# Kernel tuning notes

Hardware: AMD Instinct MI355X
Metric: run time of the kernel (lower is better)

## Reference

```python
import jax, jax.numpy as jnp
import numpy as np

B, E, H, DEPTH = 8192, 512, 512, 1


def setup_inputs() -> dict:
    key = jax.random.key(0)
    ks = jax.random.split(key, 10)
    inp = {
        "X": jax.random.normal(ks[0], (B, E), jnp.float32),
        "prev_a": jax.random.normal(ks[1], (B, DEPTH + 1, H), jnp.float32),
        "prev_b": jax.random.normal(ks[2], (B, DEPTH + 1, H), jnp.float32),
        "prev_depth": jax.random.randint(ks[3], (B, 1), 0, DEPTH + 1, jnp.int32),
        # torch.nn.Linear weights, shape [out, in], y = x @ W.T
        "w_f": jax.random.normal(ks[4], (1, H), jnp.float32) * 0.02,
        "w_a00": jax.random.normal(ks[5], (H, E + H), jnp.float32) * 0.02,
        "w_a10": jax.random.normal(ks[6], (H, E + H), jnp.float32) * 0.02,
        "w_b00": jax.random.normal(ks[7], (H, E + 2 * H), jnp.float32) * 0.02,
        "w_b11": jax.random.normal(ks[8], (H, E + H), jnp.float32) * 0.02,
        "w_b10": jax.random.normal(ks[9], (H, E + H), jnp.float32) * 0.02,
    }
    return inp


def reference(X, prev_a, prev_b, prev_depth, w_f, w_a00, w_a10, w_b00, w_b11, w_b10):
    dt = X.dtype
    # gather prev_b at current depth per batch row: prev_b[b, prev_depth[b,0], :]
    b_top = jnp.take_along_axis(prev_b, prev_depth[:, :, None], axis=1)[:, 0, :]  # [B,H]
    # fork decision; torch rounds then casts to long -> no grad flows through w_f
    f_raw = jax.lax.stop_gradient(jnp.round(jax.nn.sigmoid(b_top @ w_f.T)))  # [B,1]
    all_zero = jnp.all(prev_depth == 0)
    f = jnp.where(all_zero, jnp.ones_like(f_raw), f_raw)
    j = jnp.where(all_zero, jnp.zeros_like(f_raw), f_raw)  # else-branch sets j = f
    next_depth = prev_depth + (f - j).astype(prev_depth.dtype)  # [B,1]

    d = 1  # depth fixed to 1
    pa, pb0, pb1 = prev_a[:, d, :], prev_b[:, d - 1, :], prev_b[:, d, :]

    fj, nn_, fn = f * j, (1.0 - f) * (1.0 - j), f * (1.0 - j)  # [B,1] gates
    eq = (next_depth == d).astype(dt)
    lt = (next_depth < d).astype(dt)

    nofork_nojoin_a = jnp.concatenate([X, pa], 1) @ w_a00.T
    fork_nojoin_a = jnp.concatenate([X, pb0], 1) @ w_a10.T
    next_a1 = eq * (fj * pa + nn_ * nofork_nojoin_a + fn * fork_nojoin_a) + lt * pa

    fork_join_b = jnp.concatenate([X, pb1], 1) @ w_b11.T
    nofork_nojoin_b = jnp.concatenate([X, pa, next_a1], 1) @ w_b00.T
    fork_nojoin_b = jnp.concatenate([X, next_a1], 1) @ w_b10.T
    next_b1 = eq * (fj * fork_join_b + nn_ * nofork_nojoin_b + fn * fork_nojoin_b) + lt * pb1

    zeros = jnp.zeros_like(next_a1)
    next_a = jnp.stack([zeros, next_a1], 1)  # [B, 2, H]
    next_b = jnp.stack([zeros, next_b1], 1)  # [B, 2, H]
    return next_a, next_b, next_depth, f, j
```

## Files before the change

kernel.cpp:

```cpp
#include <hip/hip_runtime.h>
#include <hip/hip_bf16.h>

typedef __attribute__((ext_vector_type(8))) __bf16 bf16x8;
typedef __attribute__((ext_vector_type(4))) float f32x4;
typedef __attribute__((ext_vector_type(4))) unsigned short u16x4;
typedef unsigned short u16;
typedef unsigned long long u64;

typedef __attribute__((address_space(1))) void gvoid;
typedef __attribute__((address_space(3))) void lvoid;

#define B_DIM 8192
#define MFMA(a, b, c) __builtin_amdgcn_mfma_f32_16x16x32_bf16((a), (b), (c), 0, 0, 0)

__device__ __forceinline__ u16x4 cvt4(f32x4 v) {
    u16x4 r;
    r.x = __builtin_bit_cast(u16, __float2bfloat16(v.x));
    r.y = __builtin_bit_cast(u16, __float2bfloat16(v.y));
    r.z = __builtin_bit_cast(u16, __float2bfloat16(v.z));
    r.w = __builtin_bit_cast(u16, __float2bfloat16(v.w));
    return r;
}

__device__ __forceinline__ void stage64(const u16* g, int ldg, u16* ls, int t) {
#pragma unroll
    for (int it = 0; it < 2; ++it) {
        int e = it * 2048 + t * 8;
        int r = e >> 6;
        int slot = (e & 63) >> 3;
        int csrc = (slot ^ (r & 7)) << 3;
        __builtin_amdgcn_global_load_lds((gvoid*)(g + (size_t)r * ldg + csrc),
                                         (lvoid*)&ls[e], 16, 0, 0);
    }
}

__device__ __forceinline__ bf16x8 ld_frag(const u16* ls, int row, int kslot) {
    return *(const bf16x8*)&ls[row * 64 + ((kslot ^ (row & 7)) << 3)];
}

__global__ void k_dots(const float* __restrict__ prev_b, const int* __restrict__ prev_depth,
                       const float* __restrict__ w_f,
                       const float* __restrict__ wa00f, const float* __restrict__ wa10f,
                       const float* __restrict__ wb00f, const float* __restrict__ wb11f,
                       const float* __restrict__ wb10f,
                       u16* __restrict__ wa00b, u16* __restrict__ wa10b,
                       u16* __restrict__ wb00b, u16* __restrict__ wb11b,
                       u16* __restrict__ wb10b,
                       float* __restrict__ dotv) {
    int blk = blockIdx.x;
    if (blk >= 2048) {
        int t = (blk - 2048) * 256 + threadIdx.x;
        const int S = 131072, SB = 196608;
        const float* src; u16* dst; int off;
        if      (t < S)            { src = wa00f; dst = wa00b; off = t; }
        else if (t < 2 * S)        { src = wa10f; dst = wa10b; off = t - S; }
        else if (t < 2 * S + SB)   { src = wb00f; dst = wb00b; off = t - 2 * S; }
        else if (t < 3 * S + SB)   { src = wb11f; dst = wb11b; off = t - 2 * S - SB; }
        else if (t < 4 * S + SB)   { src = wb10f; dst = wb10b; off = t - 3 * S - SB; }
        else return;
        f32x4 v = *(const f32x4*)(src + (size_t)off * 4);
        *(u16x4*)(dst + (size_t)off * 4) = cvt4(v);
        return;
    }
    int wv = threadIdx.x >> 6, l = threadIdx.x & 63;
    int row = blk * 4 + wv;
    int depth = prev_depth[row];
    const float* bt = prev_b + (size_t)row * 1024 + (size_t)depth * 512;
    const int i1 = l * 4, i2 = 256 + l * 4;
    f32x4 v0 = *(const f32x4*)(bt + i1);
    f32x4 v1 = *(const f32x4*)(bt + i2);
    f32x4 w0 = *(const f32x4*)(w_f + i1);
    f32x4 w1 = *(const f32x4*)(w_f + i2);
    float dot = v0.x*w0.x + v0.y*w0.y + v0.z*w0.z + v0.w*w0.w
              + v1.x*w1.x + v1.y*w1.y + v1.z*w1.z + v1.w*w1.w;
    for (int off = 32; off > 0; off >>= 1) dot += __shfl_xor(dot, off, 64);
    if (l == 0) dotv[row] = dot;
}

__global__ __launch_bounds__(1024) void k_scan(
        const float* __restrict__ dotv, const int* __restrict__ prev_depth,
        int* __restrict__ info, int* __restrict__ idx, int* __restrict__ cnt) {
    __shared__ u64 wtot[16];
    __shared__ int wany[16];
    const int tid = threadIdx.x, lane = tid & 63, wv = tid >> 6;
    int r0 = tid * 8;
    int dep[8]; float dv[8];
    int any = 0;
#pragma unroll
    for (int r = 0; r < 8; ++r) {
        dep[r] = prev_depth[r0 + r];
        dv[r] = dotv[r0 + r];
        any |= dep[r];
    }
    for (int off = 32; off > 0; off >>= 1) any |= __shfl_xor(any, off, 64);
    if (lane == 0) wany[wv] = any;
    __syncthreads();
    int ga = 0;
#pragma unroll
    for (int w = 0; w < 16; ++w) ga |= wany[w];
    int az = (ga == 0);

    int rcls[8], rf[8], rj[8], rnd[8];
    u64 pk = 0;
#pragma unroll
    for (int r = 0; r < 8; ++r) {
        float sg = 1.0f / (1.0f + expf(-dv[r]));
        int fi = (int)rintf(sg);
        int f = az ? 1 : fi;
        int j = az ? 0 : fi;
        int nd = dep[r] + f - j;
        int cls;
        if (nd == 1)     cls = f ? (j ? 2 : 1) : 0;
        else             cls = (nd < 1) ? 3 : 4;
        rcls[r] = cls; rf[r] = f; rj[r] = j; rnd[r] = nd;
        if (cls < 3) pk += 1ull << (cls * 21);
    }
    u64 own = pk;
    for (int off = 1; off < 64; off <<= 1) {
        u64 v = __shfl_up(pk, off, 64);
        if (lane >= off) pk += v;
    }
    if (lane == 63) wtot[wv] = pk;
    __syncthreads();
    u64 wbase = 0, tot = 0;
#pragma unroll
    for (int w = 0; w < 16; ++w) {
        u64 v = wtot[w];
        if (w < wv) wbase += v;
        tot += v;
    }
    u64 excl = wbase + pk - own;
    const u64 M21 = (1ull << 21) - 1;
    int tot0 = (int)(tot & M21), tot1 = (int)((tot >> 21) & M21), tot2 = (int)((tot >> 42) & M21);
    int base0 = 0;
    int base1 = (tot0 + 63) & ~63;
    int base2 = base1 + ((tot1 + 63) & ~63);
    int o0 = base0 + (int)(excl & M21);
    int o1 = base1 + (int)((excl >> 21) & M21);
    int o2 = base2 + (int)((excl >> 42) & M21);
#pragma unroll
    for (int r = 0; r < 8; ++r) {
        int row = r0 + r, cls = rcls[r], pos = 0;
        if (cls == 0)      { pos = o0++; idx[pos] = row; }
        else if (cls == 1) { pos = o1++; idx[pos] = row; }
        else if (cls == 2) { pos = o2++; idx[pos] = row; }
        info[row] = cls | (rf[r] << 3) | (rj[r] << 4) | (rnd[r] << 5) | (pos << 7);
    }
    if (tid < 64) {
        int p0 = tot0 + tid;          if (p0 < base1) idx[p0] = 0;
        int p1 = base1 + tot1 + tid;  if (p1 < base2) idx[p1] = 0;
        int end2 = base2 + ((tot2 + 63) & ~63);
        int p2 = base2 + tot2 + tid;  if (p2 < end2) idx[p2] = 0;
    }
    if (tid == 0) {
        cnt[0] = tot0; cnt[1] = tot1; cnt[2] = tot2;
        cnt[4] = base0; cnt[5] = base1; cnt[6] = base2;
    }
}

__global__ void k_mid(const float* __restrict__ X, const float* __restrict__ prev_a,
                      const float* __restrict__ prev_b,
                      const int* __restrict__ info, const int* __restrict__ idx,
                      const int* __restrict__ cnt,
                      u16* __restrict__ A_all,
                      float* __restrict__ outA, float* __restrict__ outB,
                      float* __restrict__ outD, float* __restrict__ outF,
                      float* __restrict__ outJ) {
    int blk = (int)blockIdx.x;
    int wv = threadIdx.x >> 6, l = threadIdx.x & 63;
    const int i1 = l * 4, i2 = 256 + l * 4;
    if (blk >= 2048) {
        int p = (blk - 2048) * 4 + wv;
        int base1 = cnt[5], base2 = cnt[6];
        int end2 = base2 + ((cnt[2] + 63) & ~63);
        if (p >= end2) return;
        const float* sec = (p < base1) ? (prev_a + 512)
                         : (p < base2) ? prev_b
                                       : (prev_b + 512);
        int row = idx[p];
        size_t r512 = (size_t)row * 512, r1024 = (size_t)row * 1024;
        f32x4 xa = *(const f32x4*)(X + r512 + i1);
        f32x4 xb = *(const f32x4*)(X + r512 + i2);
        f32x4 sa = *(const f32x4*)(sec + r1024 + i1);
        f32x4 sb = *(const f32x4*)(sec + r1024 + i2);
        size_t pbase = (size_t)p * 1024;
        *(u16x4*)(A_all + pbase + i1)       = cvt4(xa);
        *(u16x4*)(A_all + pbase + i2)       = cvt4(xb);
        *(u16x4*)(A_all + pbase + 512 + i1) = cvt4(sa);
        *(u16x4*)(A_all + pbase + 512 + i2) = cvt4(sb);
        return;
    }
    int row = blk * 4 + wv;
    int inf = info[row];
    int cls = inf & 7;
    size_t r1024 = (size_t)row * 1024;
    f32x4 z; z.x = 0.f; z.y = 0.f; z.z = 0.f; z.w = 0.f;
    *(f32x4*)(outA + r1024 + i1) = z;
    *(f32x4*)(outA + r1024 + i2) = z;
    *(f32x4*)(outB + r1024 + i1) = z;
    *(f32x4*)(outB + r1024 + i2) = z;
    if (l == 0) {
        outD[row] = (float)((inf >> 5) & 3);
        outF[row] = (float)((inf >> 3) & 1);
        outJ[row] = (float)((inf >> 4) & 1);
    }
    if (cls == 2 || cls == 3) {
        f32x4 pa0 = *(const f32x4*)(prev_a + r1024 + 512 + i1);
        f32x4 pa1 = *(const f32x4*)(prev_a + r1024 + 512 + i2);
        *(f32x4*)(outA + r1024 + 512 + i1) = pa0;
        *(f32x4*)(outA + r1024 + 512 + i2) = pa1;
        if (cls == 3) {
            f32x4 q10 = *(const f32x4*)(prev_b + r1024 + 512 + i1);
            f32x4 q11 = *(const f32x4*)(prev_b + r1024 + 512 + i2);
            *(f32x4*)(outB + r1024 + 512 + i1) = q10;
            *(f32x4*)(outB + r1024 + 512 + i2) = q11;
        }
    } else if (cls == 4) {
        *(f32x4*)(outA + r1024 + 512 + i1) = z;
        *(f32x4*)(outA + r1024 + 512 + i2) = z;
        *(f32x4*)(outB + r1024 + 512 + i1) = z;
        *(f32x4*)(outB + r1024 + 512 + i2) = z;
    }
}

__global__ __launch_bounds__(256, 4) void k_s1(
    const u16* __restrict__ A_all,
    const u16* __restrict__ wa00, const u16* __restrict__ wa10,
    const u16* __restrict__ wb00, const u16* __restrict__ wb11,
    const u16* __restrict__ wb10,
    const int* __restrict__ idx, const int* __restrict__ cnt,
    u16* __restrict__ na1_all, float* __restrict__ part,
    float* __restrict__ outA, float* __restrict__ outB)
{
    __shared__ u16 lsA[4096], lsB0[4096], lsB1[4096];
    int c0 = cnt[0], c1 = cnt[1], c2 = cnt[2];
    int base0 = cnt[4], base1 = cnt[5], base2 = cnt[6];
    int t0 = (c0 + 63) >> 6, t1 = (c1 + 63) >> 6, t2 = (c2 + 63) >> 6;
    int blk = (int)blockIdx.x;
    int T = blk >> 3, nt = blk & 7;
    int cls, mb, cc;
    const u16 *W0, *W1 = nullptr;
    int ldW1 = 0;
    if (T < t0)                { cls = 0; mb = base0 + T * 64; cc = c0; W0 = wa00; W1 = wb00; ldW1 = 1536; }
    else if (T < t0 + t1)      { T -= t0; cls = 1; mb = base1 + T * 64; cc = c1; W0 = wa10; W1 = wb10; ldW1 = 1024; }
    else if (T < t0 + t1 + t2) { T -= t0 + t1; cls = 2; mb = base2 + T * 64; cc = c2; W0 = wb11; }
    else return;
    const int t = threadIdx.x;
    const int n0 = nt * 64;
    const int lane = t & 63, wv = t >> 6;
    const int wr = (wv >> 1) * 32, wc = (wv & 1) * 32;
    const int fr = lane & 15, fq = lane >> 4;

    f32x4 acc0[2][2] = {}, acc1[2][2] = {};

    for (int kq = 0; kq < 16; ++kq) {
        int cb = kq * 64;
        stage64(A_all + (size_t)mb * 1024 + cb, 1024, lsA, t);
        stage64(W0 + (size_t)n0 * 1024 + cb, 1024, lsB0, t);
        bool dual = (cls == 0) || (cls == 1 && kq < 8);
        if (dual) stage64(W1 + (size_t)n0 * ldW1 + cb, ldW1, lsB1, t);
        __syncthreads();
#pragma unroll
        for (int kk = 0; kk < 2; ++kk) {
            int ks = kk * 4 + fq;
            bf16x8 a[2], b0[2], b1[2];
#pragma unroll
            for (int mi = 0; mi < 2; ++mi) a[mi] = ld_frag(lsA, wr + mi * 16 + fr, ks);
#pragma unroll
            for (int ni = 0; ni < 2; ++ni) b0[ni] = ld_frag(lsB0, wc + ni * 16 + fr, ks);
            if (dual) {
#pragma unroll
                for (int ni = 0; ni < 2; ++ni) b1[ni] = ld_frag(lsB1, wc + ni * 16 + fr, ks);
            }
#pragma unroll
            for (int mi = 0; mi < 2; ++mi)
#pragma unroll
                for (int ni = 0; ni < 2; ++ni) {
                    acc0[mi][ni] = MFMA(a[mi], b0[ni], acc0[mi][ni]);
                    if (dual) acc1[mi][ni] = MFMA(a[mi], b1[ni], acc1[mi][ni]);
                }
        }
        __syncthreads();
    }
    int lt0 = T * 64;
#pragma unroll
    for (int mi = 0; mi < 2; ++mi)
#pragma unroll
        for (int jj = 0; jj < 4; ++jj) {
            int lr = wr + mi * 16 + fq * 4 + jj;
            if (lt0 + lr >= cc) continue;
            int grow = idx[mb + lr];
#pragma unroll
            for (int ni = 0; ni < 2; ++ni) {
                int col = n0 + wc + ni * 16 + fr;
                float v = acc0[mi][ni][jj];
                if (cls < 2) {
                    na1_all[(size_t)(mb + lr) * 512 + col] = __builtin_bit_cast(u16, __float2bfloat16(v));
                    outA[(size_t)grow * 1024 + 512 + col] = v;
                    part[(size_t)(mb + lr) * 512 + col] = acc1[mi][ni][jj];
                } else {
                    outB[(size_t)grow * 1024 + 512 + col] = v;
                }
            }
        }
}

__global__ __launch_bounds__(256, 4) void k_s2(
    const u16* __restrict__ na1_all,
    const u16* __restrict__ wb00, const u16* __restrict__ wb10,
    const int* __restrict__ idx, const int* __restrict__ cnt,
    const float* __restrict__ part, float* __restrict__ outB)
{
    __shared__ u16 lsA[4096], lsB[4096];
    int c0 = cnt[0], c1 = cnt[1];
    int base0 = cnt[4], base1 = cnt[5];
    int t0 = (c0 + 63) >> 6, t1 = (c1 + 63) >> 6;
    int blk = (int)blockIdx.x;
    int T = blk >> 3, nt = blk & 7;
    int mb, cc, ldW, kofs;
    const u16* W;
    if (T < t0)           { mb = base0 + T * 64; cc = c0; W = wb00; ldW = 1536; kofs = 1024; }
    else if (T < t0 + t1) { T -= t0; mb = base1 + T * 64; cc = c1; W = wb10; ldW = 1024; kofs = 512; }
    else return;
    const int t = threadIdx.x;
    const int n0 = nt * 64;
    const int lane = t & 63, wv = t >> 6;
    const int wr = (wv >> 1) * 32, wc = (wv & 1) * 32;
    const int fr = lane & 15, fq = lane >> 4;

    f32x4 acc[2][2];
#pragma unroll
    for (int mi = 0; mi < 2; ++mi)
#pragma unroll
        for (int ni = 0; ni < 2; ++ni)
#pragma unroll
            for (int jj = 0; jj < 4; ++jj)
                acc[mi][ni][jj] = part[(size_t)(mb + wr + mi * 16 + fq * 4 + jj) * 512
                                       + n0 + wc + ni * 16 + fr];

    for (int kq = 0; kq < 8; ++kq) {
        stage64(na1_all + (size_t)mb * 512 + kq * 64, 512, lsA, t);
        stage64(W + (size_t)n0 * ldW + kofs + kq * 64, ldW, lsB, t);
        __syncthreads();
#pragma unroll
        for (int kk = 0; kk < 2; ++kk) {
            int ks = kk * 4 + fq;
            bf16x8 a[2], b[2];
#pragma unroll
            for (int mi = 0; mi < 2; ++mi) a[mi] = ld_frag(lsA, wr + mi * 16 + fr, ks);
#pragma unroll
            for (int ni = 0; ni < 2; ++ni) b[ni] = ld_frag(lsB, wc + ni * 16 + fr, ks);
#pragma unroll
            for (int mi = 0; mi < 2; ++mi)
#pragma unroll
                for (int ni = 0; ni < 2; ++ni)
                    acc[mi][ni] = MFMA(a[mi], b[ni], acc[mi][ni]);
        }
        __syncthreads();
    }
    int lt0 = T * 64;
#pragma unroll
    for (int mi = 0; mi < 2; ++mi)
#pragma unroll
        for (int jj = 0; jj < 4; ++jj) {
            int lr = wr + mi * 16 + fq * 4 + jj;
            if (lt0 + lr >= cc) continue;
            int grow = idx[mb + lr];
#pragma unroll
            for (int ni = 0; ni < 2; ++ni) {
                int col = n0 + wc + ni * 16 + fr;
                outB[(size_t)grow * 1024 + 512 + col] = acc[mi][ni][jj];
            }
        }
}

extern "C" void kernel_launch(void* const* d_in, const int* in_sizes, int n_in,
                              void* d_out, int out_size, void* d_ws, size_t ws_size,
                              hipStream_t stream) {
    const float* X          = (const float*)d_in[0];
    const float* prev_a     = (const float*)d_in[1];
    const float* prev_b     = (const float*)d_in[2];
    const int*   prev_depth = (const int*)d_in[3];
    const float* w_f        = (const float*)d_in[4];
    const float* w_a00      = (const float*)d_in[5];
    const float* w_a10      = (const float*)d_in[6];
    const float* w_b00      = (const float*)d_in[7];
    const float* w_b11      = (const float*)d_in[8];
    const float* w_b10      = (const float*)d_in[9];

    float* out  = (float*)d_out;
    float* outA = out;
    float* outB = out + 8388608;
    float* outD = out + 16777216;
    float* outF = outD + 8192;
    float* outJ = outF + 8192;

    char* ws = (char*)d_ws;
    size_t off = 0;
    auto alloc = [&](size_t bytes) -> char* {
        char* p = ws + off;
        off += (bytes + 255) & ~(size_t)255;
        return p;
    };
    const int ROWS = 8448;
    u16* A_all    = (u16*)alloc((size_t)ROWS * 1024 * 2);
    u16* na1_all  = (u16*)alloc((size_t)ROWS * 512 * 2);
    float* part   = (float*)alloc((size_t)ROWS * 512 * 4);
    u16* wa00b = (u16*)alloc((size_t)512 * 1024 * 2);
    u16* wa10b = (u16*)alloc((size_t)512 * 1024 * 2);
    u16* wb00b = (u16*)alloc((size_t)512 * 1536 * 2);
    u16* wb11b = (u16*)alloc((size_t)512 * 1024 * 2);
    u16* wb10b = (u16*)alloc((size_t)512 * 1024 * 2);
    float* dotv = (float*)alloc((size_t)B_DIM * 4);
    int* info   = (int*)alloc((size_t)B_DIM * 4);
    int* idx    = (int*)alloc((size_t)ROWS * 4);
    int* cnt    = (int*)alloc(256);
    if (off > ws_size) return;

    k_dots<<<4864, 256, 0, stream>>>(prev_b, prev_depth, w_f,
                                     w_a00, w_a10, w_b00, w_b11, w_b10,
                                     wa00b, wa10b, wb00b, wb11b, wb10b, dotv);
    k_scan<<<1, 1024, 0, stream>>>(dotv, prev_depth, info, idx, cnt);
    k_mid<<<4128, 256, 0, stream>>>(X, prev_a, prev_b, info, idx, cnt,
                                    A_all, outA, outB, outD, outF, outJ);
    k_s1<<<1040, 256, 0, stream>>>(A_all, wa00b, wa10b, wb00b, wb11b, wb10b,
                                   idx, cnt, na1_all, part, outA, outB);
    k_s2<<<1040, 256, 0, stream>>>(na1_all, wb00b, wb10b, idx, cnt, part, outB);
}
```

Before: 65.73 us.

## Redistribute output writes across kernels to shrink the gather stage

Zeroing the depth-0 output slices moves into the dot-product kernel, which already walks each row. The per-row copies, depth/fork/join writes and class-4 zeroing move from the gather kernel into extra blocks appended to the first GEMM kernel. The gather kernel is left with only the bf16 operand packing, which shortens the critical path before the GEMM. The row-wise copy traffic now runs alongside the GEMM blocks, at the cost of a larger grid and possible contention with GEMM memory traffic.

```diff
diff --git a/kernel.cpp b/kernel.cpp
--- a/kernel.cpp
+++ b/kernel.cpp
@@ -46,7 +46,8 @@
                        u16* __restrict__ wa00b, u16* __restrict__ wa10b,
                        u16* __restrict__ wb00b, u16* __restrict__ wb11b,
                        u16* __restrict__ wb10b,
-                       float* __restrict__ dotv) {
+                       float* __restrict__ dotv,
+                       float* __restrict__ outA, float* __restrict__ outB) {
     int blk = blockIdx.x;
     if (blk >= 2048) {
         int t = (blk - 2048) * 256 + threadIdx.x;
@@ -74,6 +75,12 @@
     float dot = v0.x*w0.x + v0.y*w0.y + v0.z*w0.z + v0.w*w0.w
               + v1.x*w1.x + v1.y*w1.y + v1.z*w1.z + v1.w*w1.w;
     for (int off = 32; off > 0; off >>= 1) dot += __shfl_xor(dot, off, 64);
+    size_t r1024 = (size_t)row * 1024;
+    f32x4 z; z.x = 0.f; z.y = 0.f; z.z = 0.f; z.w = 0.f;
+    *(f32x4*)(outA + r1024 + i1) = z;
+    *(f32x4*)(outA + r1024 + i2) = z;
+    *(f32x4*)(outB + r1024 + i1) = z;
+    *(f32x4*)(outB + r1024 + i2) = z;
     if (l == 0) dotv[row] = dot;
 }
 
@@ -160,67 +167,28 @@
 
 __global__ void k_mid(const float* __restrict__ X, const float* __restrict__ prev_a,
                       const float* __restrict__ prev_b,
-                      const int* __restrict__ info, const int* __restrict__ idx,
-                      const int* __restrict__ cnt,
-                      u16* __restrict__ A_all,
-                      float* __restrict__ outA, float* __restrict__ outB,
-                      float* __restrict__ outD, float* __restrict__ outF,
-                      float* __restrict__ outJ) {
-    int blk = (int)blockIdx.x;
+                      const int* __restrict__ idx, const int* __restrict__ cnt,
+                      u16* __restrict__ A_all) {
     int wv = threadIdx.x >> 6, l = threadIdx.x & 63;
     const int i1 = l * 4, i2 = 256 + l * 4;
-    if (blk >= 2048) {
-        int p = (blk - 2048) * 4 + wv;
-        int base1 = cnt[5], base2 = cnt[6];
-        int end2 = base2 + ((cnt[2] + 63) & ~63);
-        if (p >= end2) return;
-        const float* sec = (p < base1) ? (prev_a + 512)
-                         : (p < base2) ? prev_b
-                                       : (prev_b + 512);
-        int row = idx[p];
-        size_t r512 = (size_t)row * 512, r1024 = (size_t)row * 1024;
-        f32x4 xa = *(const f32x4*)(X + r512 + i1);
-        f32x4 xb = *(const f32x4*)(X + r512 + i2);
-        f32x4 sa = *(const f32x4*)(sec + r1024 + i1);
-        f32x4 sb = *(const f32x4*)(sec + r1024 + i2);
-        size_t pbase = (size_t)p * 1024;
-        *(u16x4*)(A_all + pbase + i1)       = cvt4(xa);
-        *(u16x4*)(A_all + pbase + i2)       = cvt4(xb);
-        *(u16x4*)(A_all + pbase + 512 + i1) = cvt4(sa);
-        *(u16x4*)(A_all + pbase + 512 + i2) = cvt4(sb);
-        return;
-    }
-    int row = blk * 4 + wv;
-    int inf = info[row];
-    int cls = inf & 7;
-    size_t r1024 = (size_t)row * 1024;
-    f32x4 z; z.x = 0.f; z.y = 0.f; z.z = 0.f; z.w = 0.f;
-    *(f32x4*)(outA + r1024 + i1) = z;
-    *(f32x4*)(outA + r1024 + i2) = z;
-    *(f32x4*)(outB + r1024 + i1) = z;
-    *(f32x4*)(outB + r1024 + i2) = z;
-    if (l == 0) {
-        outD[row] = (float)((inf >> 5) & 3);
-        outF[row] = (float)((inf >> 3) & 1);
-        outJ[row] = (float)((inf >> 4) & 1);
-    }
-    if (cls == 2 || cls == 3) {
-        f32x4 pa0 = *(const f32x4*)(prev_a + r1024 + 512 + i1);
-        f32x4 pa1 = *(const f32x4*)(prev_a + r1024 + 512 + i2);
-        *(f32x4*)(outA + r1024 + 512 + i1) = pa0;
-        *(f32x4*)(outA + r1024 + 512 + i2) = pa1;
-        if (cls == 3) {
-            f32x4 q10 = *(const f32x4*)(prev_b + r1024 + 512 + i1);
-            f32x4 q11 = *(const f32x4*)(prev_b + r1024 + 512 + i2);
-            *(f32x4*)(outB + r1024 + 512 + i1) = q10;
-            *(f32x4*)(outB + r1024 + 512 + i2) = q11;
-        }
-    } else if (cls == 4) {
-        *(f32x4*)(outA + r1024 + 512 + i1) = z;
-        *(f32x4*)(outA + r1024 + 512 + i2) = z;
-        *(f32x4*)(outB + r1024 + 512 + i1) = z;
-        *(f32x4*)(outB + r1024 + 512 + i2) = z;
-    }
+    int p = (int)blockIdx.x * 4 + wv;
+    int base1 = cnt[5], base2 = cnt[6];
+    int end2 = base2 + ((cnt[2] + 63) & ~63);
+    if (p >= end2) return;
+    const float* sec = (p < base1) ? (prev_a + 512)
+                     : (p < base2) ? prev_b
+                                   : (prev_b + 512);
+    int row = idx[p];
+    size_t r512 = (size_t)row * 512, r1024 = (size_t)row * 1024;
+    f32x4 xa = *(const f32x4*)(X + r512 + i1);
+    f32x4 xb = *(const f32x4*)(X + r512 + i2);
+    f32x4 sa = *(const f32x4*)(sec + r1024 + i1);
+    f32x4 sb = *(const f32x4*)(sec + r1024 + i2);
+    size_t pbase = (size_t)p * 1024;
+    *(u16x4*)(A_all + pbase + i1)       = cvt4(xa);
+    *(u16x4*)(A_all + pbase + i2)       = cvt4(xb);
+    *(u16x4*)(A_all + pbase + 512 + i1) = cvt4(sa);
+    *(u16x4*)(A_all + pbase + 512 + i2) = cvt4(sb);
 }
 
 __global__ __launch_bounds__(256, 4) void k_s1(
@@ -228,15 +196,50 @@
     const u16* __restrict__ wa00, const u16* __restrict__ wa10,
     const u16* __restrict__ wb00, const u16* __restrict__ wb11,
     const u16* __restrict__ wb10,
-    const int* __restrict__ idx, const int* __restrict__ cnt,
+    const int* __restrict__ idx, const int* __restrict__ cnt, const int* __restrict__ info,
+    const float* __restrict__ prev_a, const float* __restrict__ prev_b,
     u16* __restrict__ na1_all, float* __restrict__ part,
-    float* __restrict__ outA, float* __restrict__ outB)
+    float* __restrict__ outA, float* __restrict__ outB,
+    float* __restrict__ outD, float* __restrict__ outF, float* __restrict__ outJ)
 {
     __shared__ u16 lsA[4096], lsB0[4096], lsB1[4096];
+    int blk = (int)blockIdx.x;
+    if (blk >= 1040) {
+        int pb_ = blk - 1040;
+        int wv = threadIdx.x >> 6, l = threadIdx.x & 63;
+        int row = pb_ * 4 + wv;
+        int inf = info[row];
+        int cls = inf & 7;
+        size_t r1024 = (size_t)row * 1024;
+        const int i1 = l * 4, i2 = 256 + l * 4;
+        if (l == 0) {
+            outD[row] = (float)((inf >> 5) & 3);
+            outF[row] = (float)((inf >> 3) & 1);
+            outJ[row] = (float)((inf >> 4) & 1);
+        }
+        if (cls == 2 || cls == 3) {
+            f32x4 pa0 = *(const f32x4*)(prev_a + r1024 + 512 + i1);
+            f32x4 pa1 = *(const f32x4*)(prev_a + r1024 + 512 + i2);
+            *(f32x4*)(outA + r1024 + 512 + i1) = pa0;
+            *(f32x4*)(outA + r1024 + 512 + i2) = pa1;
+            if (cls == 3) {
+                f32x4 q10 = *(const f32x4*)(prev_b + r1024 + 512 + i1);
+                f32x4 q11 = *(const f32x4*)(prev_b + r1024 + 512 + i2);
+                *(f32x4*)(outB + r1024 + 512 + i1) = q10;
+                *(f32x4*)(outB + r1024 + 512 + i2) = q11;
+            }
+        } else if (cls == 4) {
+            f32x4 z; z.x = 0.f; z.y = 0.f; z.z = 0.f; z.w = 0.f;
+            *(f32x4*)(outA + r1024 + 512 + i1) = z;
+            *(f32x4*)(outA + r1024 + 512 + i2) = z;
+            *(f32x4*)(outB + r1024 + 512 + i1) = z;
+            *(f32x4*)(outB + r1024 + 512 + i2) = z;
+        }
+        return;
+    }
     int c0 = cnt[0], c1 = cnt[1], c2 = cnt[2];
     int base0 = cnt[4], base1 = cnt[5], base2 = cnt[6];
     int t0 = (c0 + 63) >> 6, t1 = (c1 + 63) >> 6, t2 = (c2 + 63) >> 6;
-    int blk = (int)blockIdx.x;
     int T = blk >> 3, nt = blk & 7;
     int cls, mb, cc;
     const u16 *W0, *W1 = nullptr;
@@ -419,11 +422,12 @@
 
     k_dots<<<4864, 256, 0, stream>>>(prev_b, prev_depth, w_f,
                                      w_a00, w_a10, w_b00, w_b11, w_b10,
-                                     wa00b, wa10b, wb00b, wb11b, wb10b, dotv);
+                                     wa00b, wa10b, wb00b, wb11b, wb10b,
+                                     dotv, outA, outB);
     k_scan<<<1, 1024, 0, stream>>>(dotv, prev_depth, info, idx, cnt);
-    k_mid<<<4128, 256, 0, stream>>>(X, prev_a, prev_b, info, idx, cnt,
-                                    A_all, outA, outB, outD, outF, outJ);
-    k_s1<<<1040, 256, 0, stream>>>(A_all, wa00b, wa10b, wb00b, wb11b, wb10b,
-                                   idx, cnt, na1_all, part, outA, outB);
+    k_mid<<<2080, 256, 0, stream>>>(X, prev_a, prev_b, idx, cnt, A_all);
+    k_s1<<<3088, 256, 0, stream>>>(A_all, wa00b, wa10b, wb00b, wb11b, wb10b,
+                                   idx, cnt, info, prev_a, prev_b,
+                                   na1_all, part, outA, outB, outD, outF, outJ);
     k_s2<<<1040, 256, 0, stream>>>(na1_all, wb00b, wb10b, idx, cnt, part, outB);
 }
```

Result: faster. 63.59 us (-3.3%).
